# Kernel optimization log

Hardware: AMD Instinct MI355X
Metric: run time of the kernel (lower is better)

## Reference

```python
import jax, jax.numpy as jnp
import numpy as np
from jax import lax

K = 3       # kernel_conv
STRIDE = 1
PAD = 1


def setup_inputs() -> dict:
    key = jax.random.key(0)
    ks = jax.random.split(key, 11)
    b, n, H, W = 8, 64, 128, 128
    m = 64
    kk = K * K
    return {
        "x": jax.random.normal(ks[0], (b, n, H, W), jnp.float32),
        "atw1": jax.random.uniform(ks[1], (b, kk, H, W), jnp.float32),  # sigmoid-range attention1 output
        "weight": jax.random.normal(ks[2], (m, n, K, K), jnp.float32) * 0.05,
        "a2_w1": jax.random.normal(ks[3], (kk, n), jnp.float32) * 0.1,
        "a2_b1": jax.random.normal(ks[4], (kk,), jnp.float32) * 0.1,
        "a2_w2": jax.random.normal(ks[5], (kk, kk), jnp.float32) * 0.1,
        "a2_b2": jax.random.normal(ks[6], (kk,), jnp.float32) * 0.1,
        "a3_w1": jax.random.normal(ks[7], (m, n), jnp.float32) * 0.1,
        "a3_b1": jax.random.normal(ks[8], (m,), jnp.float32) * 0.1,
        "a3_w2": jax.random.normal(ks[9], (m, m), jnp.float32) * 0.1,
        "a3_b2": jax.random.normal(ks[10], (m,), jnp.float32) * 0.1,
    }


def reference(x, atw1, weight, a2_w1, a2_b1, a2_w2, a2_b2, a3_w1, a3_b1, a3_w2, a3_b2):
    b, n, H, W = x.shape
    m = weight.shape[0]
    kk = K * K
    n_H = 1 + (H + 2 * PAD - K) // STRIDE
    n_W = 1 + (W + 2 * PAD - K) // STRIDE
    P = n_H * n_W

    # F.unfold(x, k, stride, padding): [b, n*k*k, P] with channel-major ordering (c, kh, kw)
    patches = lax.conv_general_dilated_patches(
        x, (K, K), (STRIDE, STRIDE), [(PAD, PAD), (PAD, PAD)])  # [b, n*kk, n_H, n_W]
    kx = patches.reshape(b, n, kk, P)

    # attention2: global avg pool + two 1x1 convs -> per-batch per-tap ratio [b, kk]
    g = x.mean(axis=(2, 3))                                   # [b, n]
    ratio = jax.nn.relu(g @ a2_w1.T + a2_b1) @ a2_w2.T + a2_b2  # [b, kk]

    # per-pixel per-tap weight (broadcast over input channels, as the torch repeat/view does)
    a = atw1.reshape(b, kk, P) * ratio[:, :, None]            # [b, kk, P]
    wx = kx * a[:, None, :, :]                                # [b, n, kk, P]

    # dynamic-weighted im2col matmul with static conv weight
    w = weight.reshape(m, n, kk)
    y = jnp.einsum('bctp,mct->bmp', wx, w)                    # [b, m, P]

    # attention3 bias: global avg pool + two 1x1 convs -> [b, m]
    bias = jax.nn.relu(g @ a3_w1.T + a3_b1) @ a3_w2.T + a3_b2
    y = y + bias[:, :, None]

    # F.fold with kernel 1 is a reshape back to the spatial grid
    return y.reshape(b, m, n_H, n_W)
```

## Files before the change

kernel.cpp:

```cpp
#include <hip/hip_runtime.h>

typedef __attribute__((ext_vector_type(8))) short short8;
typedef __attribute__((ext_vector_type(4))) float f32x4;

#define HH 128
#define WW 128
#define TW 16
#define TH 4
#define HALOW 18
#define HALOH 6
#define NPIX (HALOW * HALOH)
#define NGROUP (TH / 2)

__device__ inline unsigned short f2bf(float f) {
    unsigned int u = __builtin_bit_cast(unsigned int, f);
    u += 0x7fffu + ((u >> 16) & 1u);
    return (unsigned short)(u >> 16);
}

__global__ __launch_bounds__(256) void mean_wprep_kernel(
    const float* __restrict__ x, const float* __restrict__ wgt,
    float* __restrict__ g, unsigned short* __restrict__ W3) {
    {
        int i = blockIdx.x * 256 + threadIdx.x;
        if (i < 64 * 64 * 9) {
            int j = i & 7, rest = i >> 3;
            int m = rest & 63; rest >>= 6;
            int lk = rest & 3; rest >>= 2;
            int ks = rest & 1, t = rest >> 1;
            int c = ks * 32 + lk * 8 + j;
            W3[i] = f2bf(wgt[(m * 64 + c) * 9 + t]);
        }
    }
    int bn = blockIdx.x;
    const float4* x4 = (const float4*)(x + (size_t)bn * (HH * WW));
    int tid = threadIdx.x;
    float s = 0.f;
    for (int i = tid; i < HH * WW / 4; i += 256) {
        float4 v = x4[i];
        s += v.x + v.y + v.z + v.w;
    }
    #pragma unroll
    for (int off = 32; off > 0; off >>= 1) s += __shfl_down(s, off, 64);
    __shared__ float wsum[4];
    int lane = tid & 63, wv = tid >> 6;
    if (lane == 0) wsum[wv] = s;
    __syncthreads();
    if (tid == 0) {
        float t = wsum[0] + wsum[1] + wsum[2] + wsum[3];
        g[bn] = t * (1.f / (HH * WW));
    }
}

__global__ __launch_bounds__(64) void mlp_kernel(
    const float* __restrict__ g,
    const float* __restrict__ a2w1, const float* __restrict__ a2b1,
    const float* __restrict__ a2w2, const float* __restrict__ a2b2,
    const float* __restrict__ a3w1, const float* __restrict__ a3b1,
    const float* __restrict__ a3w2, const float* __restrict__ a3b2,
    float* __restrict__ ratio, float* __restrict__ bias) {
    int b = blockIdx.x;
    int t = threadIdx.x;
    __shared__ float gs[64], h2[9], h3[64];
    gs[t] = g[b * 64 + t];
    __syncthreads();
    float s = 0.f;
    #pragma unroll 8
    for (int i = 0; i < 64; ++i) s += gs[i] * a3w1[t * 64 + i];
    h3[t] = fmaxf(s + a3b1[t], 0.f);
    if (t < 9) {
        float s2 = 0.f;
        #pragma unroll 8
        for (int i = 0; i < 64; ++i) s2 += gs[i] * a2w1[t * 64 + i];
        h2[t] = fmaxf(s2 + a2b1[t], 0.f);
    }
    __syncthreads();
    float o = 0.f;
    #pragma unroll 8
    for (int i = 0; i < 64; ++i) o += h3[i] * a3w2[t * 64 + i];
    bias[b * 64 + t] = o + a3b2[t];
    if (t < 9) {
        float r = 0.f;
        #pragma unroll
        for (int i = 0; i < 9; ++i) r += h2[i] * a2w2[t * 9 + i];
        ratio[b * 9 + t] = r + a2b2[t];
    }
}

__global__ __launch_bounds__(256, 4) void main_kernel(
    const float* __restrict__ x, const float* __restrict__ atw1,
    const unsigned short* __restrict__ W3, const float* __restrict__ ratio,
    const float* __restrict__ bias, float* __restrict__ out) {
    const int id = blockIdx.x;
    const int b = id & 7;
    const int rem = id >> 3;
    const int tY = rem >> 3;
    const int tX = rem & 7;
    const int tid = threadIdx.x;
    const int lane = tid & 63;
    const int wtile = tid >> 6;
    const int lm = lane & 15;
    const int lk = lane >> 4;
    const int px0 = tX * TW, py0 = tY * TH;

    __shared__ char xsc[NPIX * 128];
    __shared__ float alds[9][TH][TW];

    {
        const int sbase = wtile * 2;
        const size_t xb = (size_t)b * 64 * (HH * WW);
        #pragma unroll
        for (int pixb = 0; pixb < NPIX; pixb += 64) {
            int pix = pixb + lane;
            if (pix < NPIX) {
                int yy = pix / HALOW;
                int xx = pix - yy * HALOW;
                int gy = py0 + yy - 1, gx = px0 + xx - 1;
                bool inb = (gy >= 0) && (gy < HH) && (gx >= 0) && (gx < WW);
                int sp = gy * WW + gx;
                #pragma unroll
                for (int s2 = 0; s2 < 2; ++s2) {
                    int s = sbase + s2;
                    unsigned int pk[4];
                    #pragma unroll
                    for (int j2 = 0; j2 < 4; ++j2) {
                        float v0 = 0.f, v1 = 0.f;
                        if (inb) {
                            v0 = x[xb + (size_t)(s * 8 + j2 * 2) * (HH * WW) + sp];
                            v1 = x[xb + (size_t)(s * 8 + j2 * 2 + 1) * (HH * WW) + sp];
                        }
                        pk[j2] = (unsigned)f2bf(v0) | ((unsigned)f2bf(v1) << 16);
                    }
                    *(uint4*)(xsc + pix * 128 + ((s * 16) ^ ((pix & 7) << 4))) =
                        make_uint4(pk[0], pk[1], pk[2], pk[3]);
                }
            }
        }
    }

    #pragma unroll
    for (int i = tid; i < 9 * TH * TW; i += 256) {
        int t = i / (TH * TW);
        int rem2 = i - t * (TH * TW);
        int rr = rem2 >> 4, cc = rem2 & 15;
        alds[0][0][i] = atw1[((size_t)(b * 9 + t) * HH + py0 + rr) * WW + px0 + cc]
                        * ratio[b * 9 + t];
    }

    short8 wfrag[9][2];
    {
        const short8* W3v = (const short8*)W3;
        #pragma unroll
        for (int t = 0; t < 9; ++t)
            #pragma unroll
            for (int ks = 0; ks < 2; ++ks)
                wfrag[t][ks] = W3v[(((t * 2 + ks) * 4 + lk) * 64) + wtile * 16 + lm];
    }

    float biasr[4];
    #pragma unroll
    for (int q = 0; q < 4; ++q) biasr[q] = bias[b * 64 + wtile * 16 + lk * 4 + q];

    __syncthreads();

    #pragma unroll 1
    for (int g2 = 0; g2 < NGROUP; ++g2) {
        const int r0 = g2 * 2;
        float av[2][9];
        #pragma unroll
        for (int rr = 0; rr < 2; ++rr)
            #pragma unroll
            for (int t = 0; t < 9; ++t) av[rr][t] = alds[t][r0 + rr][lm];

        f32x4 yac[2];
        #pragma unroll
        for (int rr = 0; rr < 2; ++rr) yac[rr] = (f32x4){0.f, 0.f, 0.f, 0.f};

        #pragma unroll
        for (int hl = 0; hl < 4; ++hl) {
            const int pixr = (r0 + hl) * HALOW + lm;
            short8 bf[3][2];
            #pragma unroll
            for (int dx = 0; dx < 3; ++dx) {
                const int pix = pixr + dx;
                const int sw = (pix & 7) << 4;
                const char* bp2 = xsc + pix * 128;
                #pragma unroll
                for (int ks = 0; ks < 2; ++ks)
                    bf[dx][ks] = __builtin_bit_cast(short8,
                        *(const uint4*)(bp2 + ((ks * 64 + lk * 16) ^ sw)));
            }
            #pragma unroll
            for (int dy = 0; dy < 3; ++dy) {
                const int r = hl - dy;
                if (r < 0 || r > 1) continue;
                #pragma unroll
                for (int dx = 0; dx < 3; ++dx) {
                    const int t = dy * 3 + dx;
                    f32x4 z = {0.f, 0.f, 0.f, 0.f};
                    z = __builtin_amdgcn_mfma_f32_16x16x32_bf16(wfrag[t][0], bf[dx][0], z, 0, 0, 0);
                    z = __builtin_amdgcn_mfma_f32_16x16x32_bf16(wfrag[t][1], bf[dx][1], z, 0, 0, 0);
                    #pragma unroll
                    for (int q = 0; q < 4; ++q) yac[r][q] = fmaf(av[r][t], z[q], yac[r][q]);
                }
            }
        }
        #pragma unroll
        for (int rr = 0; rr < 2; ++rr) {
            const int pyg = py0 + r0 + rr;
            #pragma unroll
            for (int q = 0; q < 4; ++q) {
                int m = wtile * 16 + lk * 4 + q;
                out[((size_t)(b * 64 + m) * HH + pyg) * WW + px0 + lm] = yac[rr][q] + biasr[q];
            }
        }
    }
}

extern "C" void kernel_launch(void* const* d_in, const int* in_sizes, int n_in,
                              void* d_out, int out_size, void* d_ws, size_t ws_size,
                              hipStream_t stream) {
    const float* x    = (const float*)d_in[0];
    const float* atw1 = (const float*)d_in[1];
    const float* wgt  = (const float*)d_in[2];
    const float* a2w1 = (const float*)d_in[3];
    const float* a2b1 = (const float*)d_in[4];
    const float* a2w2 = (const float*)d_in[5];
    const float* a2b2 = (const float*)d_in[6];
    const float* a3w1 = (const float*)d_in[7];
    const float* a3b1 = (const float*)d_in[8];
    const float* a3w2 = (const float*)d_in[9];
    const float* a3b2 = (const float*)d_in[10];
    float* out = (float*)d_out;

    float* ws    = (float*)d_ws;
    float* g     = ws;
    float* ratio = ws + 512;
    float* bias  = ws + 584;
    unsigned short* W3 = (unsigned short*)(ws + 1152);

    mean_wprep_kernel<<<dim3(512), dim3(256), 0, stream>>>(x, wgt, g, W3);
    mlp_kernel<<<dim3(8), dim3(64), 0, stream>>>(g, a2w1, a2b1, a2w2, a2b2,
                                                 a3w1, a3b1, a3w2, a3b2, ratio, bias);
    main_kernel<<<dim3(2048), dim3(256), 0, stream>>>(x, atw1, W3, ratio, bias, out);
}
```

Measured before the change: 44.15 us.

## Pre-transpose x to channel-last bf16 in prep kernel and fuse mean partials

The prep kernel now converts x into a channel-last bf16 buffer (xT) through an LDS transpose. While doing so it writes per-tile channel sums, which the MLP kernel reduces to get the global mean. The main kernel then fills its halo tile with 16-byte vector loads from xT, replacing strided per-channel fp32 gathers and the bf16 conversion it used to repeat for every halo. This adds an extra write and read of a 16 MB bf16 intermediate. The mean is now computed from bf16-rounded values, which costs some precision.

```diff
diff --git a/kernel.cpp b/kernel.cpp
--- a/kernel.cpp
+++ b/kernel.cpp
@@ -18,11 +18,14 @@
     return (unsigned short)(u >> 16);
 }
 
-__global__ __launch_bounds__(256) void mean_wprep_kernel(
+__global__ __launch_bounds__(256) void prep_kernel(
     const float* __restrict__ x, const float* __restrict__ wgt,
-    float* __restrict__ g, unsigned short* __restrict__ W3) {
+    unsigned short* __restrict__ xT, float* __restrict__ partials,
+    unsigned short* __restrict__ W3) {
+    const int id = blockIdx.x;
+    const int tid = threadIdx.x;
     {
-        int i = blockIdx.x * 256 + threadIdx.x;
+        int i = id * 256 + tid;
         if (i < 64 * 64 * 9) {
             int j = i & 7, rest = i >> 3;
             int m = rest & 63; rest >>= 6;
@@ -32,63 +35,100 @@
             W3[i] = f2bf(wgt[(m * 64 + c) * 9 + t]);
         }
     }
-    int bn = blockIdx.x;
-    const float4* x4 = (const float4*)(x + (size_t)bn * (HH * WW));
-    int tid = threadIdx.x;
-    float s = 0.f;
-    for (int i = tid; i < HH * WW / 4; i += 256) {
-        float4 v = x4[i];
-        s += v.x + v.y + v.z + v.w;
-    }
-    #pragma unroll
-    for (int off = 32; off > 0; off >>= 1) s += __shfl_down(s, off, 64);
-    __shared__ float wsum[4];
-    int lane = tid & 63, wv = tid >> 6;
-    if (lane == 0) wsum[wv] = s;
-    __syncthreads();
-    if (tid == 0) {
-        float t = wsum[0] + wsum[1] + wsum[2] + wsum[3];
-        g[bn] = t * (1.f / (HH * WW));
-    }
-}
-
-__global__ __launch_bounds__(64) void mlp_kernel(
-    const float* __restrict__ g,
+    const int b = id & 7, pt = id >> 3;
+    const int p0 = pt * 64;
+    __shared__ unsigned int lt[64 * 33];
+    __shared__ float red[8][32][2];
+
+    const int px = tid & 63, cp0 = tid >> 6;
+    const float* xb = x + (size_t)b * 64 * (HH * WW) + p0 + px;
+    #pragma unroll
+    for (int i = 0; i < 8; ++i) {
+        int cp = cp0 + 4 * i;
+        float v0 = xb[(size_t)(2 * cp) * (HH * WW)];
+        float v1 = xb[(size_t)(2 * cp + 1) * (HH * WW)];
+        lt[px * 33 + cp] = (unsigned)f2bf(v0) | ((unsigned)f2bf(v1) << 16);
+    }
+    __syncthreads();
+    #pragma unroll
+    for (int it = 0; it < 2; ++it) {
+        int idx = it * 256 + tid;
+        int p = idx >> 3, ch = idx & 7;
+        int o = p * 33 + ch * 4;
+        uint4 v = make_uint4(lt[o], lt[o + 1], lt[o + 2], lt[o + 3]);
+        *(uint4*)(xT + ((size_t)(b * (HH * WW) + p0 + p) * 64 + ch * 8)) = v;
+    }
+    {
+        int cp = tid & 31, grp = tid >> 5;
+        float s0 = 0.f, s1 = 0.f;
+        #pragma unroll
+        for (int j2 = 0; j2 < 8; ++j2) {
+            unsigned u = lt[(grp * 8 + j2) * 33 + cp];
+            s0 += __builtin_bit_cast(float, u << 16);
+            s1 += __builtin_bit_cast(float, u & 0xffff0000u);
+        }
+        red[grp][cp][0] = s0;
+        red[grp][cp][1] = s1;
+    }
+    __syncthreads();
+    if (tid < 64) {
+        float s = 0.f;
+        #pragma unroll
+        for (int g2 = 0; g2 < 8; ++g2) s += red[g2][tid >> 1][tid & 1];
+        partials[(size_t)(b * 256 + pt) * 64 + tid] = s;
+    }
+}
+
+__global__ __launch_bounds__(256) void mlp_kernel(
+    const float* __restrict__ partials,
     const float* __restrict__ a2w1, const float* __restrict__ a2b1,
     const float* __restrict__ a2w2, const float* __restrict__ a2b2,
     const float* __restrict__ a3w1, const float* __restrict__ a3b1,
     const float* __restrict__ a3w2, const float* __restrict__ a3b2,
     float* __restrict__ ratio, float* __restrict__ bias) {
     int b = blockIdx.x;
-    int t = threadIdx.x;
-    __shared__ float gs[64], h2[9], h3[64];
-    gs[t] = g[b * 64 + t];
-    __syncthreads();
+    int tid = threadIdx.x;
+    int t = tid & 63, is = tid >> 6;
     float s = 0.f;
     #pragma unroll 8
-    for (int i = 0; i < 64; ++i) s += gs[i] * a3w1[t * 64 + i];
-    h3[t] = fmaxf(s + a3b1[t], 0.f);
-    if (t < 9) {
-        float s2 = 0.f;
+    for (int k = 0; k < 64; ++k)
+        s += partials[(size_t)(b * 256 + is + 4 * k) * 64 + t];
+    __shared__ float rb[4][64];
+    __shared__ float gs[64], h2[9], h3[64];
+    rb[is][t] = s;
+    __syncthreads();
+    if (tid < 64)
+        gs[t] = (rb[0][t] + rb[1][t] + rb[2][t] + rb[3][t]) * (1.f / (HH * WW));
+    __syncthreads();
+    if (tid < 64) {
+        float s3 = 0.f;
         #pragma unroll 8
-        for (int i = 0; i < 64; ++i) s2 += gs[i] * a2w1[t * 64 + i];
-        h2[t] = fmaxf(s2 + a2b1[t], 0.f);
-    }
-    __syncthreads();
-    float o = 0.f;
-    #pragma unroll 8
-    for (int i = 0; i < 64; ++i) o += h3[i] * a3w2[t * 64 + i];
-    bias[b * 64 + t] = o + a3b2[t];
-    if (t < 9) {
-        float r = 0.f;
-        #pragma unroll
-        for (int i = 0; i < 9; ++i) r += h2[i] * a2w2[t * 9 + i];
-        ratio[b * 9 + t] = r + a2b2[t];
+        for (int i = 0; i < 64; ++i) s3 += gs[i] * a3w1[t * 64 + i];
+        h3[t] = fmaxf(s3 + a3b1[t], 0.f);
+        if (t < 9) {
+            float s2 = 0.f;
+            #pragma unroll 8
+            for (int i = 0; i < 64; ++i) s2 += gs[i] * a2w1[t * 64 + i];
+            h2[t] = fmaxf(s2 + a2b1[t], 0.f);
+        }
+    }
+    __syncthreads();
+    if (tid < 64) {
+        float o = 0.f;
+        #pragma unroll 8
+        for (int i = 0; i < 64; ++i) o += h3[i] * a3w2[t * 64 + i];
+        bias[b * 64 + t] = o + a3b2[t];
+        if (t < 9) {
+            float r = 0.f;
+            #pragma unroll
+            for (int i = 0; i < 9; ++i) r += h2[i] * a2w2[t * 9 + i];
+            ratio[b * 9 + t] = r + a2b2[t];
+        }
     }
 }
 
 __global__ __launch_bounds__(256, 4) void main_kernel(
-    const float* __restrict__ x, const float* __restrict__ atw1,
+    const unsigned short* __restrict__ xT, const float* __restrict__ atw1,
     const unsigned short* __restrict__ W3, const float* __restrict__ ratio,
     const float* __restrict__ bias, float* __restrict__ out) {
     const int id = blockIdx.x;
@@ -106,35 +146,18 @@
     __shared__ char xsc[NPIX * 128];
     __shared__ float alds[9][TH][TW];
 
-    {
-        const int sbase = wtile * 2;
-        const size_t xb = (size_t)b * 64 * (HH * WW);
-        #pragma unroll
-        for (int pixb = 0; pixb < NPIX; pixb += 64) {
-            int pix = pixb + lane;
-            if (pix < NPIX) {
-                int yy = pix / HALOW;
-                int xx = pix - yy * HALOW;
-                int gy = py0 + yy - 1, gx = px0 + xx - 1;
-                bool inb = (gy >= 0) && (gy < HH) && (gx >= 0) && (gx < WW);
-                int sp = gy * WW + gx;
-                #pragma unroll
-                for (int s2 = 0; s2 < 2; ++s2) {
-                    int s = sbase + s2;
-                    unsigned int pk[4];
-                    #pragma unroll
-                    for (int j2 = 0; j2 < 4; ++j2) {
-                        float v0 = 0.f, v1 = 0.f;
-                        if (inb) {
-                            v0 = x[xb + (size_t)(s * 8 + j2 * 2) * (HH * WW) + sp];
-                            v1 = x[xb + (size_t)(s * 8 + j2 * 2 + 1) * (HH * WW) + sp];
-                        }
-                        pk[j2] = (unsigned)f2bf(v0) | ((unsigned)f2bf(v1) << 16);
-                    }
-                    *(uint4*)(xsc + pix * 128 + ((s * 16) ^ ((pix & 7) << 4))) =
-                        make_uint4(pk[0], pk[1], pk[2], pk[3]);
-                }
-            }
+    #pragma unroll
+    for (int it = 0; it < 4; ++it) {
+        int idx = it * 256 + tid;
+        if (idx < NPIX * 8) {
+            int pix = idx >> 3, ch = idx & 7;
+            int yy = pix / HALOW;
+            int xx = pix - yy * HALOW;
+            int gy = py0 + yy - 1, gx = px0 + xx - 1;
+            uint4 v = make_uint4(0u, 0u, 0u, 0u);
+            if (gy >= 0 && gy < HH && gx >= 0 && gx < WW)
+                v = *(const uint4*)(xT + ((size_t)((b * HH + gy) * WW + gx) * 64 + ch * 8));
+            *(uint4*)(xsc + pix * 128 + ((ch * 16) ^ ((pix & 7) << 4))) = v;
         }
     }
 
@@ -233,14 +256,15 @@
     const float* a3b2 = (const float*)d_in[10];
     float* out = (float*)d_out;
 
-    float* ws    = (float*)d_ws;
-    float* g     = ws;
-    float* ratio = ws + 512;
-    float* bias  = ws + 584;
-    unsigned short* W3 = (unsigned short*)(ws + 1152);
-
-    mean_wprep_kernel<<<dim3(512), dim3(256), 0, stream>>>(x, wgt, g, W3);
-    mlp_kernel<<<dim3(8), dim3(64), 0, stream>>>(g, a2w1, a2b1, a2w2, a2b2,
-                                                 a3w1, a3b1, a3w2, a3b2, ratio, bias);
-    main_kernel<<<dim3(2048), dim3(256), 0, stream>>>(x, atw1, W3, ratio, bias, out);
-}
+    float* ws = (float*)d_ws;
+    float* ratio = ws;
+    float* bias  = ws + 128;
+    unsigned short* W3 = (unsigned short*)(ws + 1024);
+    float* partials = ws + 19456;
+    unsigned short* xT = (unsigned short*)(ws + 150528);
+
+    prep_kernel<<<dim3(2048), dim3(256), 0, stream>>>(x, wgt, xT, partials, W3);
+    mlp_kernel<<<dim3(8), dim3(256), 0, stream>>>(partials, a2w1, a2b1, a2w2, a2b2,
+                                                  a3w1, a3b1, a3w2, a3b2, ratio, bias);
+    main_kernel<<<dim3(2048), dim3(256), 0, stream>>>(xT, atw1, W3, ratio, bias, out);
+}
```

After: 44.04 us. No clear change (-0.3%).
